# Optimization experiments

Measured on AMD Instinct MI355X. Metric: run time of the kernel, lower is better.

The kernel has to match this reference:

```python
import jax, jax.numpy as jnp
import numpy as np

N_NODES = 100000
N_EDGES = 3200000
NFEAT = 128
NHID = 128
NCLASS = 8
BN_EPS = 1e-5


def setup_inputs() -> dict:
    key = jax.random.key(0)
    ks = jax.random.split(key, 8)
    x = jax.random.normal(ks[0], (N_NODES, NFEAT), dtype=jnp.float32)
    edge_index = jax.random.randint(ks[1], (2, N_EDGES), 0, N_NODES, dtype=jnp.int64)
    # GCNConv params: weight [nfeat, nhid] (glorot), bias [nhid]
    lim = float(np.sqrt(6.0 / (NFEAT + NHID)))
    W = jax.random.uniform(ks[2], (NFEAT, NHID), minval=-lim, maxval=lim, dtype=jnp.float32)
    b_gc = jnp.zeros((NHID,), dtype=jnp.float32)
    # BatchNorm1d params
    gamma = jnp.ones((NHID,), dtype=jnp.float32)
    beta = jnp.zeros((NHID,), dtype=jnp.float32)
    # fc head: (nhid/2) -> nclass, xavier_uniform, zero bias
    lim2 = float(np.sqrt(6.0 / (NHID // 2 + NCLASS)))
    fc_w = jax.random.uniform(ks[3], (NCLASS, NHID // 2), minval=-lim2, maxval=lim2, dtype=jnp.float32)
    fc_b = jnp.zeros((NCLASS,), dtype=jnp.float32)
    return {"x": x, "edge_index": edge_index, "W": W, "b_gc": b_gc,
            "gamma": gamma, "beta": beta, "fc_w": fc_w, "fc_b": fc_b}


def _gcn_conv(x, edge_index, W, b):
    """PyG GCNConv: add self-loops, symmetric norm, linear, gather-scatter, bias."""
    N = x.shape[0]
    loops = jnp.arange(N, dtype=edge_index.dtype)
    src = jnp.concatenate([edge_index[0], loops])  # source (row / x_j)
    dst = jnp.concatenate([edge_index[1], loops])  # target (col / aggregation index)
    # degree of target nodes (edge weight = 1)
    deg = jax.ops.segment_sum(jnp.ones_like(dst, dtype=x.dtype), dst, num_segments=N)
    dinv = jnp.where(deg > 0, jax.lax.rsqrt(deg), 0.0)
    norm = dinv[src] * dinv[dst]  # [E+N]
    h = x @ W  # [N, nhid]
    msg = h[src] * norm[:, None]  # gather + scale
    out = jax.ops.segment_sum(msg, dst, num_segments=N)  # scatter-add
    return out + b


def _batchnorm(h, gamma, beta):
    mean = jnp.mean(h, axis=0)
    var = jnp.mean(jnp.square(h - mean), axis=0)  # biased, training-mode
    return gamma * (h - mean) * jax.lax.rsqrt(var + BN_EPS) + beta


def reference(x, edge_index, W, b_gc, gamma, beta, fc_w, fc_b):
    h = _gcn_conv(x, edge_index, W, b_gc)
    embed = _batchnorm(h, gamma, beta)
    half = embed.shape[1] // 2
    out = embed[:, :half] @ fc_w.T + fc_b
    return (out, embed)
```

## Files before the change

kernel.cpp:

```cpp
#include <hip/hip_runtime.h>
#include <hip/hip_bf16.h>
#include <math.h>

#define N_NODES 100000
#define N_EDGES 3200000
#define NFEAT 128
#define NHID 128
#define NCLASS 8
#define BN_EPS 1e-5f
#define NBC 391
#define PART_BLOCKS 782
#define WT_BLOCKS 64

typedef __attribute__((ext_vector_type(8))) short short8;
typedef __attribute__((ext_vector_type(4))) float f32x4;

__device__ __forceinline__ short f2bf(float f) {
    __hip_bfloat16 b = __float2bfloat16(f);
    return *reinterpret_cast<short*>(&b);
}
__device__ __forceinline__ float bf_lo(unsigned u) { return __uint_as_float(u << 16); }
__device__ __forceinline__ float bf_hi(unsigned u) { return __uint_as_float(u & 0xffff0000u); }


__global__ __launch_bounds__(256) void k_chist(const int* __restrict__ dst,
                                               int* __restrict__ ghist,
                                               const float* __restrict__ W,
                                               unsigned short* __restrict__ Wt,
                                               uint4* __restrict__ hbz) {
    if (blockIdx.x >= PART_BLOCKS) {
        int idx = (blockIdx.x - PART_BLOCKS) * 256 + threadIdx.x;
        if (idx < 16) hbz[idx] = (uint4){0u, 0u, 0u, 0u};
        int k = idx >> 7, n = idx & 127;
        Wt[n * NFEAT + k] = (unsigned short)f2bf(W[idx]);
        return;
    }
    __shared__ int lh[NBC];
    const int tid = threadIdx.x;
    for (int i = tid; i < NBC; i += 256) lh[i] = 0;
    __syncthreads();
    const int4* dst4 = (const int4*)dst;
    const int q0 = blockIdx.x * 1024 + tid;
#pragma unroll
    for (int i = 0; i < 4; ++i) {
        int q = q0 + i * 256;
        if (q < N_EDGES / 4) {
            int4 d = dst4[q];
            atomicAdd(&lh[d.x >> 8], 1);
            atomicAdd(&lh[d.y >> 8], 1);
            atomicAdd(&lh[d.z >> 8], 1);
            atomicAdd(&lh[d.w >> 8], 1);
        }
    }
    __syncthreads();
    for (int i = tid; i < NBC; i += 256) {
        int c = lh[i];
        if (c) atomicAdd(&ghist[i], c);
    }
}

__global__ __launch_bounds__(512) void k_cscan(const int* __restrict__ ghist,
                                               int* __restrict__ coff,
                                               int* __restrict__ ccur,
                                               int* __restrict__ off,
                                               float* __restrict__ stats,
                                               int* __restrict__ ticket) {
    __shared__ int tmp[512];
    const int t = threadIdx.x;
    if (t < 256) stats[t] = 0.f;
    if (t == 0) *ticket = 0;
    int v = (t < NBC) ? ghist[t] : 0;
    tmp[t] = v;
    __syncthreads();
    for (int d = 1; d < 512; d <<= 1) {
        int u = (t >= d) ? tmp[t - d] : 0;
        __syncthreads();
        tmp[t] += u;
        __syncthreads();
    }
    int excl = tmp[t] - v;
    if (t < NBC) {
        coff[t] = excl;
        ccur[t] = excl;
    }
    if (t == NBC - 1) {
        coff[NBC] = tmp[t];
        off[N_NODES] = tmp[t];
    }
}

__global__ __launch_bounds__(256) void k_part(const int* __restrict__ src,
                                              const int* __restrict__ dst,
                                              int* __restrict__ ccur,
                                              unsigned* __restrict__ epack) {
    __shared__ int lh[NBC];
    __shared__ int lbase[NBC];
    const int tid = threadIdx.x;
    for (int i = tid; i < NBC; i += 256) lh[i] = 0;
    __syncthreads();
    const int4* src4 = (const int4*)src;
    const int4* dst4 = (const int4*)dst;
    const int q0 = blockIdx.x * 1024 + tid;
    int4 sv[4], dv[4];
    int rk[16];
    bool val[4];
#pragma unroll
    for (int i = 0; i < 4; ++i) {
        int q = q0 + i * 256;
        val[i] = q < N_EDGES / 4;
        if (val[i]) {
            sv[i] = src4[q];
            dv[i] = dst4[q];
            rk[i * 4 + 0] = atomicAdd(&lh[dv[i].x >> 8], 1);
            rk[i * 4 + 1] = atomicAdd(&lh[dv[i].y >> 8], 1);
            rk[i * 4 + 2] = atomicAdd(&lh[dv[i].z >> 8], 1);
            rk[i * 4 + 3] = atomicAdd(&lh[dv[i].w >> 8], 1);
        }
    }
    __syncthreads();
    for (int i = tid; i < NBC; i += 256) {
        int c = lh[i];
        lbase[i] = c ? atomicAdd(&ccur[i], c) : 0;
    }
    __syncthreads();
#pragma unroll
    for (int i = 0; i < 4; ++i) {
        if (val[i]) {
            epack[lbase[dv[i].x >> 8] + rk[i * 4 + 0]] = ((unsigned)sv[i].x << 8) | (unsigned)(dv[i].x & 255);
            epack[lbase[dv[i].y >> 8] + rk[i * 4 + 1]] = ((unsigned)sv[i].y << 8) | (unsigned)(dv[i].y & 255);
            epack[lbase[dv[i].z >> 8] + rk[i * 4 + 2]] = ((unsigned)sv[i].z << 8) | (unsigned)(dv[i].z & 255);
            epack[lbase[dv[i].w >> 8] + rk[i * 4 + 3]] = ((unsigned)sv[i].w << 8) | (unsigned)(dv[i].w & 255);
        }
    }
}

__global__ __launch_bounds__(256) void k_fine(const unsigned* __restrict__ epack,
                                              const int* __restrict__ coff,
                                              int* __restrict__ off,
                                              float* __restrict__ dinv,
                                              int* __restrict__ esrc) {
    __shared__ int lh[256], lcur[256], lsc[256];
    const int tid = threadIdx.x;
    const int b = blockIdx.x;
    const int node0 = b << 8;
    const int span = min(256, N_NODES - node0);
    lh[tid] = 0;
    __syncthreads();
    const int lo = coff[b], hiEnd = coff[b + 1];
    for (int i = lo + tid; i < hiEnd; i += 256)
        atomicAdd(&lh[epack[i] & 255u], 1);
    __syncthreads();
    int v = lh[tid];
    lsc[tid] = v;
    __syncthreads();
    for (int d = 1; d < 256; d <<= 1) {
        int u = (tid >= d) ? lsc[tid - d] : 0;
        __syncthreads();
        lsc[tid] += u;
        __syncthreads();
    }
    int excl = lsc[tid] - v;
    lcur[tid] = excl;
    if (tid < span) {
        off[node0 + tid] = lo + excl;
        dinv[node0 + tid] = rsqrtf((float)(v + 1));
    }
    __syncthreads();
    for (int i = lo + tid; i < hiEnd; i += 256) {
        unsigned p = epack[i];
        int pos = atomicAdd(&lcur[p & 255u], 1);
        esrc[lo + pos] = (int)(p >> 8);
    }
}


#define WSTRIDE 136
__global__ __launch_bounds__(256) void k_gemm(const float* __restrict__ x,
                                              const unsigned short* __restrict__ Wt,
                                              const float* __restrict__ dinv,
                                              unsigned short* __restrict__ hb) {
    __shared__ short wlds[NHID * WSTRIDE];
    const int tid = threadIdx.x;

    const unsigned* Wt32 = (const unsigned*)Wt;
    unsigned* wl32 = (unsigned*)wlds;
#pragma unroll
    for (int i = 0; i < 32; ++i) {
        int d = tid + i * 256;
        int n = d >> 6, kp = d & 63;
        wl32[n * (WSTRIDE / 2) + kp] = Wt32[d];
    }
    __syncthreads();

    const int wid = tid >> 6, lane = tid & 63;
    const int qw = lane >> 4, lr = lane & 15;
    const int arow = blockIdx.x * 64 + wid * 16 + lr;
    const bool avalid = arow < N_NODES;

    short8 a[4];
#pragma unroll
    for (int ks = 0; ks < 4; ++ks) {
        if (avalid) {
            const float* p = x + (size_t)arow * NFEAT + ks * 32 + qw * 8;
            float4 v0 = *(const float4*)p;
            float4 v1 = *(const float4*)(p + 4);
            short8 t;
            t[0] = f2bf(v0.x); t[1] = f2bf(v0.y); t[2] = f2bf(v0.z); t[3] = f2bf(v0.w);
            t[4] = f2bf(v1.x); t[5] = f2bf(v1.y); t[6] = f2bf(v1.z); t[7] = f2bf(v1.w);
            a[ks] = t;
        } else {
            short8 t;
#pragma unroll
            for (int j = 0; j < 8; ++j) t[j] = 0;
            a[ks] = t;
        }
    }

    f32x4 acc[8];
#pragma unroll
    for (int nt = 0; nt < 8; ++nt) acc[nt] = (f32x4){0.f, 0.f, 0.f, 0.f};

#pragma unroll
    for (int nt = 0; nt < 8; ++nt) {
#pragma unroll
        for (int ks = 0; ks < 4; ++ks) {
            short8 bfr = *(const short8*)&wlds[(nt * 16 + lr) * WSTRIDE + ks * 32 + qw * 8];
            acc[nt] = __builtin_amdgcn_mfma_f32_16x16x32_bf16(a[ks], bfr, acc[nt], 0, 0, 0);
        }
    }

    const int rbase = blockIdx.x * 64 + wid * 16 + qw * 4;
    float dv[4];
#pragma unroll
    for (int j = 0; j < 4; ++j) dv[j] = (rbase + j < N_NODES) ? dinv[rbase + j] : 0.f;
#pragma unroll
    for (int j = 0; j < 4; ++j) {
        int r = rbase + j;
        if (r >= N_NODES) continue;
#pragma unroll
        for (int nt = 0; nt < 8; ++nt)
            hb[(size_t)r * NHID + nt * 16 + lr] = (unsigned short)f2bf(dv[j] * acc[nt][j]);
    }
}


__global__ __launch_bounds__(256) void k_agg(const int* __restrict__ off,
                                             const int* __restrict__ esrc,
                                             const float* __restrict__ dinv,
                                             const uint2* __restrict__ hbq,
                                             float4* __restrict__ agg4) {
    const int node = (blockIdx.x << 2) | (threadIdx.x >> 6);
    const int lane = threadIdx.x & 63;
    const int hl = lane >> 5;
    const int cl = lane & 31;
    if (node >= N_NODES) return;

    const float dn = dinv[node];
    const int self = hl ? N_NODES : node;
    uint2 u0 = hbq[(size_t)self * 32 + cl];
    float aAx = bf_lo(u0.x), aAy = bf_hi(u0.x), aAz = bf_lo(u0.y), aAw = bf_hi(u0.y);
    float aBx = 0.f, aBy = 0.f, aBz = 0.f, aBw = 0.f;
    float aCx = 0.f, aCy = 0.f, aCz = 0.f, aCw = 0.f;
    float aDx = 0.f, aDy = 0.f, aDz = 0.f, aDw = 0.f;

    const int begin = off[node], end = off[node + 1];
    for (int base = begin; base < end; base += 64) {
        int m = end - base;
        if (m > 64) m = 64;
        int sv = (lane < m) ? esrc[base + lane] : N_NODES;
        const int kmax = (m + 7) >> 3;
        for (int k = 0; k < kmax; ++k) {
            int sA = __shfl(sv, 8 * k + 0 + hl);
            int sB = __shfl(sv, 8 * k + 2 + hl);
            int sC = __shfl(sv, 8 * k + 4 + hl);
            int sD = __shfl(sv, 8 * k + 6 + hl);
            uint2 uA = hbq[(size_t)sA * 32 + cl];
            uint2 uB = hbq[(size_t)sB * 32 + cl];
            uint2 uC = hbq[(size_t)sC * 32 + cl];
            uint2 uD = hbq[(size_t)sD * 32 + cl];
            aAx += bf_lo(uA.x); aAy += bf_hi(uA.x); aAz += bf_lo(uA.y); aAw += bf_hi(uA.y);
            aBx += bf_lo(uB.x); aBy += bf_hi(uB.x); aBz += bf_lo(uB.y); aBw += bf_hi(uB.y);
            aCx += bf_lo(uC.x); aCy += bf_hi(uC.x); aCz += bf_lo(uC.y); aCw += bf_hi(uC.y);
            aDx += bf_lo(uD.x); aDy += bf_hi(uD.x); aDz += bf_lo(uD.y); aDw += bf_hi(uD.y);
        }
    }
    float ax = (aAx + aBx) + (aCx + aDx);
    float ay = (aAy + aBy) + (aCy + aDy);
    float az = (aAz + aBz) + (aCz + aDz);
    float aw = (aAw + aBw) + (aCw + aDw);
    ax += __shfl_xor(ax, 32);
    ay += __shfl_xor(ay, 32);
    az += __shfl_xor(az, 32);
    aw += __shfl_xor(aw, 32);
    if (hl == 0) {
        float4 o;
        o.x = ax * dn; o.y = ay * dn; o.z = az * dn; o.w = aw * dn;
        agg4[(size_t)node * 32 + cl] = o;
    }
}


__global__ __launch_bounds__(256) void k_stats(const float* __restrict__ agg,
                                               float* __restrict__ stats,
                                               int* __restrict__ ticket,
                                               const float* __restrict__ gamma,
                                               const float* __restrict__ beta,
                                               float* __restrict__ ss) {
    const int cb = threadIdx.x & 31;
    const int rg = threadIdx.x >> 5;
    const float4* a4 = (const float4*)agg;
    float4 s = {0.f, 0.f, 0.f, 0.f}, s2 = {0.f, 0.f, 0.f, 0.f};
    for (int r = blockIdx.x * 8 + rg; r < N_NODES; r += gridDim.x * 8) {
        float4 v = a4[(size_t)r * 32 + cb];
        s.x += v.x; s.y += v.y; s.z += v.z; s.w += v.w;
        s2.x += v.x * v.x; s2.y += v.y * v.y; s2.z += v.z * v.z; s2.w += v.w * v.w;
    }
    __shared__ float4 ls[256], ls2[256];
    __shared__ int lastflag;
    ls[threadIdx.x] = s;
    ls2[threadIdx.x] = s2;
    __syncthreads();
    if (rg == 0) {
        float4 ts = ls[cb], t2 = ls2[cb];
#pragma unroll
        for (int g = 1; g < 8; ++g) {
            float4 v = ls[g * 32 + cb], w = ls2[g * 32 + cb];
            ts.x += v.x; ts.y += v.y; ts.z += v.z; ts.w += v.w;
            t2.x += w.x; t2.y += w.y; t2.z += w.z; t2.w += w.w;
        }
        atomicAdd(&stats[cb * 4 + 0], ts.x);
        atomicAdd(&stats[cb * 4 + 1], ts.y);
        atomicAdd(&stats[cb * 4 + 2], ts.z);
        atomicAdd(&stats[cb * 4 + 3], ts.w);
        atomicAdd(&stats[128 + cb * 4 + 0], t2.x);
        atomicAdd(&stats[128 + cb * 4 + 1], t2.y);
        atomicAdd(&stats[128 + cb * 4 + 2], t2.z);
        atomicAdd(&stats[128 + cb * 4 + 3], t2.w);
    }
    __threadfence();
    __syncthreads();
    if (threadIdx.x == 0)
        lastflag = (atomicAdd(ticket, 1) == (int)gridDim.x - 1) ? 1 : 0;
    __syncthreads();
    if (lastflag && threadIdx.x < NHID) {
        int c = threadIdx.x;
        float sum = atomicAdd(&stats[c], 0.f);
        float sq  = atomicAdd(&stats[128 + c], 0.f);
        float mean = sum / (float)N_NODES;
        float var = fmaxf(sq / (float)N_NODES - mean * mean, 0.f);
        float inv = rsqrtf(var + BN_EPS);
        float sc = gamma[c] * inv;
        ss[c] = sc;
        ss[128 + c] = beta[c] - mean * sc;
    }
}


__global__ __launch_bounds__(256) void k_bnfc(float* __restrict__ embed,
                                              const float* __restrict__ ss,
                                              const float* __restrict__ fc_w,
                                              const float* __restrict__ fc_b,
                                              float* __restrict__ out) {
    __shared__ float se[64][68];
    __shared__ float sw[8][68];
    __shared__ float sb[8];
    const int tid = threadIdx.x;
    const int row0 = blockIdx.x * 64;
    {
        int d = tid;
        sw[d >> 6][d & 63] = fc_w[d];
        d = tid + 256;
        sw[d >> 6][d & 63] = fc_w[d];
        if (tid < 8) sb[tid] = fc_b[tid];
    }
    float4* ef4 = (float4*)embed;
    const float4* ssc4 = (const float4*)ss;
    const float4* ssh4 = (const float4*)(ss + 128);
#pragma unroll
    for (int i = 0; i < 8; ++i) {
        int d = tid + i * 256;
        int r = d >> 5;
        int cb = d & 31;
        int gr = row0 + r;
        if (gr < N_NODES) {
            float4 v = ef4[(size_t)gr * 32 + cb];
            float4 sc = ssc4[cb], sh = ssh4[cb];
            v.x = fmaf(v.x, sc.x, sh.x);
            v.y = fmaf(v.y, sc.y, sh.y);
            v.z = fmaf(v.z, sc.z, sh.z);
            v.w = fmaf(v.w, sc.w, sh.w);
            ef4[(size_t)gr * 32 + cb] = v;
            if (cb < 16) {
                se[r][cb * 4 + 0] = v.x; se[r][cb * 4 + 1] = v.y;
                se[r][cb * 4 + 2] = v.z; se[r][cb * 4 + 3] = v.w;
            }
        } else if (cb < 16) {
            se[r][cb * 4 + 0] = 0.f; se[r][cb * 4 + 1] = 0.f;
            se[r][cb * 4 + 2] = 0.f; se[r][cb * 4 + 3] = 0.f;
        }
    }
    __syncthreads();
    const int r = tid >> 2;
    const int j0 = (tid & 3) * 2;
    const int gr = row0 + r;
#pragma unroll
    for (int jj = 0; jj < 2; ++jj) {
        int j = j0 + jj;
        float s = sb[j];
#pragma unroll
        for (int k = 0; k < 64; ++k) s = fmaf(se[r][k], sw[j][k], s);
        if (gr < N_NODES) out[(size_t)gr * NCLASS + j] = s;
    }
}


extern "C" void kernel_launch(void* const* d_in, const int* in_sizes, int n_in,
                              void* d_out, int out_size, void* d_ws, size_t ws_size,
                              hipStream_t stream) {
    const float* x     = (const float*)d_in[0];
    const int*   ei    = (const int*)d_in[1];
    const float* W     = (const float*)d_in[2];
    const float* gamma = (const float*)d_in[4];
    const float* beta  = (const float*)d_in[5];
    const float* fc_w  = (const float*)d_in[6];
    const float* fc_b  = (const float*)d_in[7];

    const int* src = ei;
    const int* dst = ei + N_EDGES;

    float* out   = (float*)d_out;
    float* embed = (float*)d_out + (size_t)N_NODES * NCLASS;

    char* ws = (char*)d_ws;
    size_t o = 0;
    unsigned* epack = (unsigned*)(ws + o);          o += (size_t)N_EDGES * 4;
    unsigned short* hb = (unsigned short*)(ws + o); o += (size_t)(N_NODES + 1) * NHID * 2;
    o = (o + 255) & ~(size_t)255;
    int* esrc   = (int*)(ws + o);                   o += (size_t)N_EDGES * 4;
    int* off    = (int*)(ws + o);                   o += (size_t)(N_NODES + 1) * 4;
    float* dinv = (float*)(ws + o);                 o += (size_t)N_NODES * 4;
    unsigned short* Wt = (unsigned short*)(ws + o); o += (size_t)NFEAT * NHID * 2;
    float* stats = (float*)(ws + o);                o += 256 * 4;
    float* ss    = (float*)(ws + o);                o += 256 * 4;
    int* ghist   = (int*)(ws + o);                  o += NBC * 4;
    int* coff    = (int*)(ws + o);                  o += (NBC + 1) * 4;
    int* ccur    = (int*)(ws + o);                  o += NBC * 4;
    int* ticket  = (int*)(ws + o);                  o += 4;

    hipMemsetAsync(ghist, 0, NBC * 4, stream);

    k_chist<<<PART_BLOCKS + WT_BLOCKS, 256, 0, stream>>>(dst, ghist, W, Wt,
                                                         (uint4*)(hb + (size_t)N_NODES * NHID));
    k_cscan<<<1, 512, 0, stream>>>(ghist, coff, ccur, off, stats, ticket);
    k_part<<<PART_BLOCKS, 256, 0, stream>>>(src, dst, ccur, epack);
    k_fine<<<NBC, 256, 0, stream>>>(epack, coff, off, dinv, esrc);

    k_gemm<<<(N_NODES + 63) / 64, 256, 0, stream>>>(x, Wt, dinv, hb);

    k_agg<<<(N_NODES + 3) / 4, 256, 0, stream>>>(off, esrc, dinv, (const uint2*)hb, (float4*)embed);

    k_stats<<<512, 256, 0, stream>>>(embed, stats, ticket, gamma, beta, ss);

    k_bnfc<<<(N_NODES + 63) / 64, 256, 0, stream>>>(embed, ss, fc_w, fc_b, out);
}
```

Baseline: 321.2 us.

## Split feature matrix into 16-column slices so aggregation gathers stay cache-resident

The GEMM now writes h in eight column-slice planes of 16 bf16 features each. The aggregation kernel is reorganized so each block handles one slice for 8 nodes, with each wave gathering only 32-byte rows. The aim is to shrink the random-gather working set per slice (about 3.2 MB) so it fits in L2/LLC, improving hit rate on the 3.2M-edge gather. The cost is that the edge list is re-read eight times (with nontemporal loads) and outputs are written as strided scalar stores. Block-to-slice interleaving sets the order in which slices run.

```diff
diff --git a/kernel.cpp b/kernel.cpp
--- a/kernel.cpp
+++ b/kernel.cpp
@@ -11,6 +11,7 @@
 #define NBC 391
 #define PART_BLOCKS 782
 #define WT_BLOCKS 64
+#define PSTRIDE_U ((N_NODES + 16) * 16)
 
 typedef __attribute__((ext_vector_type(8))) short short8;
 typedef __attribute__((ext_vector_type(4))) float f32x4;
@@ -27,10 +28,13 @@
                                                int* __restrict__ ghist,
                                                const float* __restrict__ W,
                                                unsigned short* __restrict__ Wt,
-                                               uint4* __restrict__ hbz) {
+                                               unsigned short* __restrict__ hbS) {
     if (blockIdx.x >= PART_BLOCKS) {
         int idx = (blockIdx.x - PART_BLOCKS) * 256 + threadIdx.x;
-        if (idx < 16) hbz[idx] = (uint4){0u, 0u, 0u, 0u};
+        if (idx < 128) {
+            int s = idx >> 4, e = idx & 15;
+            hbS[(size_t)s * PSTRIDE_U + (size_t)N_NODES * 16 + e] = 0;
+        }
         int k = idx >> 7, n = idx & 127;
         Wt[n * NFEAT + k] = (unsigned short)f2bf(W[idx]);
         return;
@@ -178,7 +182,7 @@
 __global__ __launch_bounds__(256) void k_gemm(const float* __restrict__ x,
                                               const unsigned short* __restrict__ Wt,
                                               const float* __restrict__ dinv,
-                                              unsigned short* __restrict__ hb) {
+                                              unsigned short* __restrict__ hbS) {
     __shared__ short wlds[NHID * WSTRIDE];
     const int tid = threadIdx.x;
 
@@ -239,63 +243,55 @@
         if (r >= N_NODES) continue;
 #pragma unroll
         for (int nt = 0; nt < 8; ++nt)
-            hb[(size_t)r * NHID + nt * 16 + lr] = (unsigned short)f2bf(dv[j] * acc[nt][j]);
-    }
-}
-
-
-__global__ __launch_bounds__(256) void k_agg(const int* __restrict__ off,
+            hbS[(size_t)nt * PSTRIDE_U + (size_t)r * 16 + lr] = (unsigned short)f2bf(dv[j] * acc[nt][j]);
+    }
+}
+
+
+__global__ __launch_bounds__(512) void k_agg(const int* __restrict__ off,
                                              const int* __restrict__ esrc,
                                              const float* __restrict__ dinv,
-                                             const uint2* __restrict__ hbq,
-                                             float4* __restrict__ agg4) {
-    const int node = (blockIdx.x << 2) | (threadIdx.x >> 6);
+                                             const unsigned* __restrict__ hbS32,
+                                             float* __restrict__ embed) {
+    const int slice = blockIdx.x & 7;
+    const int chunk = blockIdx.x >> 3;
+    const int wv = threadIdx.x >> 6;
     const int lane = threadIdx.x & 63;
-    const int hl = lane >> 5;
-    const int cl = lane & 31;
-    if (node >= N_NODES) return;
-
-    const float dn = dinv[node];
-    const int self = hl ? N_NODES : node;
-    uint2 u0 = hbq[(size_t)self * 32 + cl];
-    float aAx = bf_lo(u0.x), aAy = bf_hi(u0.x), aAz = bf_lo(u0.y), aAw = bf_hi(u0.y);
-    float aBx = 0.f, aBy = 0.f, aBz = 0.f, aBw = 0.f;
-    float aCx = 0.f, aCy = 0.f, aCz = 0.f, aCw = 0.f;
-    float aDx = 0.f, aDy = 0.f, aDz = 0.f, aDw = 0.f;
+    const int grp = lane >> 3, gl = lane & 7;
+    const int node = chunk * 8 + wv;
+
+    const unsigned* __restrict__ hp = hbS32 + (size_t)slice * (PSTRIDE_U / 2);
+
+    unsigned u0 = (grp == 0) ? hp[(size_t)node * 8 + gl] : 0u;
+    float aAx = bf_lo(u0), aAy = bf_hi(u0);
+    float aBx = 0.f, aBy = 0.f;
 
     const int begin = off[node], end = off[node + 1];
     for (int base = begin; base < end; base += 64) {
         int m = end - base;
         if (m > 64) m = 64;
-        int sv = (lane < m) ? esrc[base + lane] : N_NODES;
+        int sv = (lane < m) ? __builtin_nontemporal_load(esrc + base + lane) : N_NODES;
         const int kmax = (m + 7) >> 3;
-        for (int k = 0; k < kmax; ++k) {
-            int sA = __shfl(sv, 8 * k + 0 + hl);
-            int sB = __shfl(sv, 8 * k + 2 + hl);
-            int sC = __shfl(sv, 8 * k + 4 + hl);
-            int sD = __shfl(sv, 8 * k + 6 + hl);
-            uint2 uA = hbq[(size_t)sA * 32 + cl];
-            uint2 uB = hbq[(size_t)sB * 32 + cl];
-            uint2 uC = hbq[(size_t)sC * 32 + cl];
-            uint2 uD = hbq[(size_t)sD * 32 + cl];
-            aAx += bf_lo(uA.x); aAy += bf_hi(uA.x); aAz += bf_lo(uA.y); aAw += bf_hi(uA.y);
-            aBx += bf_lo(uB.x); aBy += bf_hi(uB.x); aBz += bf_lo(uB.y); aBw += bf_hi(uB.y);
-            aCx += bf_lo(uC.x); aCy += bf_hi(uC.x); aCz += bf_lo(uC.y); aCw += bf_hi(uC.y);
-            aDx += bf_lo(uD.x); aDy += bf_hi(uD.x); aDz += bf_lo(uD.y); aDw += bf_hi(uD.y);
-        }
-    }
-    float ax = (aAx + aBx) + (aCx + aDx);
-    float ay = (aAy + aBy) + (aCy + aDy);
-    float az = (aAz + aBz) + (aCz + aDz);
-    float aw = (aAw + aBw) + (aCw + aDw);
-    ax += __shfl_xor(ax, 32);
-    ay += __shfl_xor(ay, 32);
-    az += __shfl_xor(az, 32);
-    aw += __shfl_xor(aw, 32);
-    if (hl == 0) {
-        float4 o;
-        o.x = ax * dn; o.y = ay * dn; o.z = az * dn; o.w = aw * dn;
-        agg4[(size_t)node * 32 + cl] = o;
+        for (int k = 0; k < kmax; k += 2) {
+            int sA = __shfl(sv, 8 * k + grp);
+            int sB = __shfl(sv, 8 * k + 8 + grp);
+            unsigned uA = hp[(size_t)sA * 8 + gl];
+            unsigned uB = hp[(size_t)sB * 8 + gl];
+            aAx += bf_lo(uA); aAy += bf_hi(uA);
+            aBx += bf_lo(uB); aBy += bf_hi(uB);
+        }
+    }
+    float ax = aAx + aBx, ay = aAy + aBy;
+#pragma unroll
+    for (int d = 8; d < 64; d <<= 1) {
+        ax += __shfl_xor(ax, d);
+        ay += __shfl_xor(ay, d);
+    }
+    if (grp == 0) {
+        const float dn = dinv[node];
+        float* ep = embed + (size_t)node * NHID + slice * 16 + gl * 2;
+        __builtin_nontemporal_store(ax * dn, ep);
+        __builtin_nontemporal_store(ay * dn, ep + 1);
     }
 }
 
@@ -434,7 +430,7 @@
     char* ws = (char*)d_ws;
     size_t o = 0;
     unsigned* epack = (unsigned*)(ws + o);          o += (size_t)N_EDGES * 4;
-    unsigned short* hb = (unsigned short*)(ws + o); o += (size_t)(N_NODES + 1) * NHID * 2;
+    unsigned short* hbS = (unsigned short*)(ws + o); o += (size_t)8 * PSTRIDE_U * 2;
     o = (o + 255) & ~(size_t)255;
     int* esrc   = (int*)(ws + o);                   o += (size_t)N_EDGES * 4;
     int* off    = (int*)(ws + o);                   o += (size_t)(N_NODES + 1) * 4;
@@ -449,15 +445,14 @@
 
     hipMemsetAsync(ghist, 0, NBC * 4, stream);
 
-    k_chist<<<PART_BLOCKS + WT_BLOCKS, 256, 0, stream>>>(dst, ghist, W, Wt,
-                                                         (uint4*)(hb + (size_t)N_NODES * NHID));
+    k_chist<<<PART_BLOCKS + WT_BLOCKS, 256, 0, stream>>>(dst, ghist, W, Wt, hbS);
     k_cscan<<<1, 512, 0, stream>>>(ghist, coff, ccur, off, stats, ticket);
     k_part<<<PART_BLOCKS, 256, 0, stream>>>(src, dst, ccur, epack);
     k_fine<<<NBC, 256, 0, stream>>>(epack, coff, off, dinv, esrc);
 
-    k_gemm<<<(N_NODES + 63) / 64, 256, 0, stream>>>(x, Wt, dinv, hb);
-
-    k_agg<<<(N_NODES + 3) / 4, 256, 0, stream>>>(off, esrc, dinv, (const uint2*)hb, (float4*)embed);
+    k_gemm<<<(N_NODES + 63) / 64, 256, 0, stream>>>(x, Wt, dinv, hbS);
+
+    k_agg<<<8 * (N_NODES / 8), 512, 0, stream>>>(off, esrc, dinv, (const unsigned*)hbS, embed);
 
     k_stats<<<512, 256, 0, stream>>>(embed, stats, ticket, gamma, beta, ss);
 
```

New measurement: 479.2 us. +49.2%, slower.

## Stage partitioned edges in LDS and widen coarse buckets to 512 nodes

Applied to the files above, without the earlier changes.

The coarse partition now uses 512-node buckets (196 buckets) and 8192 edges per block. Each block sorts its edges locally in shared memory by bucket, using an in-block scan, before writing them to global memory. The goal is to turn scattered 4-byte global writes into mostly contiguous runs per bucket and to halve the number of global atomics on the bucket cursors. The cost is more LDS per block (about 48KB), which lowers occupancy, plus extra scans and syncs; the fine pass also has to handle 512 nodes per block.

```diff
diff --git a/kernel.cpp b/kernel.cpp
--- a/kernel.cpp
+++ b/kernel.cpp
@@ -8,8 +8,10 @@
 #define NHID 128
 #define NCLASS 8
 #define BN_EPS 1e-5f
-#define NBC 391
-#define PART_BLOCKS 782
+#define CB 512
+#define NBC 196
+#define EPB 8192
+#define PART_BLOCKS 391
 #define WT_BLOCKS 64
 
 typedef __attribute__((ext_vector_type(8))) short short8;
@@ -37,25 +39,25 @@
     }
     __shared__ int lh[NBC];
     const int tid = threadIdx.x;
-    for (int i = tid; i < NBC; i += 256) lh[i] = 0;
+    if (tid < NBC) lh[tid] = 0;
     __syncthreads();
     const int4* dst4 = (const int4*)dst;
-    const int q0 = blockIdx.x * 1024 + tid;
-#pragma unroll
-    for (int i = 0; i < 4; ++i) {
+    const int q0 = blockIdx.x * (EPB / 4) + tid;
+#pragma unroll
+    for (int i = 0; i < 8; ++i) {
         int q = q0 + i * 256;
         if (q < N_EDGES / 4) {
             int4 d = dst4[q];
-            atomicAdd(&lh[d.x >> 8], 1);
-            atomicAdd(&lh[d.y >> 8], 1);
-            atomicAdd(&lh[d.z >> 8], 1);
-            atomicAdd(&lh[d.w >> 8], 1);
-        }
-    }
-    __syncthreads();
-    for (int i = tid; i < NBC; i += 256) {
-        int c = lh[i];
-        if (c) atomicAdd(&ghist[i], c);
+            atomicAdd(&lh[d.x >> 9], 1);
+            atomicAdd(&lh[d.y >> 9], 1);
+            atomicAdd(&lh[d.z >> 9], 1);
+            atomicAdd(&lh[d.w >> 9], 1);
+        }
+    }
+    __syncthreads();
+    if (tid < NBC) {
+        int c = lh[tid];
+        if (c) atomicAdd(&ghist[tid], c);
     }
 }
 
@@ -89,69 +91,93 @@
     }
 }
 
+
 __global__ __launch_bounds__(256) void k_part(const int* __restrict__ src,
                                               const int* __restrict__ dst,
                                               int* __restrict__ ccur,
                                               unsigned* __restrict__ epack) {
     __shared__ int lh[NBC];
-    __shared__ int lbase[NBC];
+    __shared__ int lstart[NBC];
+    __shared__ int adj[NBC];
+    __shared__ int stmp[256];
+    __shared__ unsigned sorted[EPB];
+    __shared__ unsigned short bkt[EPB];
     const int tid = threadIdx.x;
-    for (int i = tid; i < NBC; i += 256) lh[i] = 0;
+    if (tid < NBC) lh[tid] = 0;
     __syncthreads();
     const int4* src4 = (const int4*)src;
     const int4* dst4 = (const int4*)dst;
-    const int q0 = blockIdx.x * 1024 + tid;
-    int4 sv[4], dv[4];
-    int rk[16];
-    bool val[4];
-#pragma unroll
-    for (int i = 0; i < 4; ++i) {
+    const int q0 = blockIdx.x * (EPB / 4) + tid;
+    int4 sv[8], dv[8];
+    int rk[32];
+#pragma unroll
+    for (int i = 0; i < 8; ++i) {
         int q = q0 + i * 256;
-        val[i] = q < N_EDGES / 4;
-        if (val[i]) {
+        if (q < N_EDGES / 4) {
             sv[i] = src4[q];
             dv[i] = dst4[q];
-            rk[i * 4 + 0] = atomicAdd(&lh[dv[i].x >> 8], 1);
-            rk[i * 4 + 1] = atomicAdd(&lh[dv[i].y >> 8], 1);
-            rk[i * 4 + 2] = atomicAdd(&lh[dv[i].z >> 8], 1);
-            rk[i * 4 + 3] = atomicAdd(&lh[dv[i].w >> 8], 1);
-        }
-    }
-    __syncthreads();
-    for (int i = tid; i < NBC; i += 256) {
-        int c = lh[i];
-        lbase[i] = c ? atomicAdd(&ccur[i], c) : 0;
-    }
-    __syncthreads();
-#pragma unroll
-    for (int i = 0; i < 4; ++i) {
-        if (val[i]) {
-            epack[lbase[dv[i].x >> 8] + rk[i * 4 + 0]] = ((unsigned)sv[i].x << 8) | (unsigned)(dv[i].x & 255);
-            epack[lbase[dv[i].y >> 8] + rk[i * 4 + 1]] = ((unsigned)sv[i].y << 8) | (unsigned)(dv[i].y & 255);
-            epack[lbase[dv[i].z >> 8] + rk[i * 4 + 2]] = ((unsigned)sv[i].z << 8) | (unsigned)(dv[i].z & 255);
-            epack[lbase[dv[i].w >> 8] + rk[i * 4 + 3]] = ((unsigned)sv[i].w << 8) | (unsigned)(dv[i].w & 255);
-        }
-    }
-}
+            rk[i * 4 + 0] = atomicAdd(&lh[dv[i].x >> 9], 1);
+            rk[i * 4 + 1] = atomicAdd(&lh[dv[i].y >> 9], 1);
+            rk[i * 4 + 2] = atomicAdd(&lh[dv[i].z >> 9], 1);
+            rk[i * 4 + 3] = atomicAdd(&lh[dv[i].w >> 9], 1);
+        } else dv[i].x = -1;
+    }
+    __syncthreads();
+    int v = (tid < NBC) ? lh[tid] : 0;
+    stmp[tid] = v;
+    __syncthreads();
+    for (int d = 1; d < 256; d <<= 1) {
+        int u = (tid >= d) ? stmp[tid - d] : 0;
+        __syncthreads();
+        stmp[tid] += u;
+        __syncthreads();
+    }
+    if (tid < NBC) {
+        int ls = stmp[tid] - v;
+        lstart[tid] = ls;
+        adj[tid] = (v ? atomicAdd(&ccur[tid], v) : 0) - ls;
+    }
+    __syncthreads();
+#pragma unroll
+    for (int i = 0; i < 8; ++i) {
+        if (dv[i].x >= 0) {
+            int b, p;
+            b = dv[i].x >> 9; p = lstart[b] + rk[i * 4 + 0];
+            sorted[p] = ((unsigned)sv[i].x << 9) | (unsigned)(dv[i].x & 511); bkt[p] = (unsigned short)b;
+            b = dv[i].y >> 9; p = lstart[b] + rk[i * 4 + 1];
+            sorted[p] = ((unsigned)sv[i].y << 9) | (unsigned)(dv[i].y & 511); bkt[p] = (unsigned short)b;
+            b = dv[i].z >> 9; p = lstart[b] + rk[i * 4 + 2];
+            sorted[p] = ((unsigned)sv[i].z << 9) | (unsigned)(dv[i].z & 511); bkt[p] = (unsigned short)b;
+            b = dv[i].w >> 9; p = lstart[b] + rk[i * 4 + 3];
+            sorted[p] = ((unsigned)sv[i].w << 9) | (unsigned)(dv[i].w & 511); bkt[p] = (unsigned short)b;
+        }
+    }
+    __syncthreads();
+    const int vcnt = stmp[255];
+    for (int p = tid; p < vcnt; p += 256)
+        epack[p + adj[bkt[p]]] = sorted[p];
+}
+
 
 __global__ __launch_bounds__(256) void k_fine(const unsigned* __restrict__ epack,
                                               const int* __restrict__ coff,
                                               int* __restrict__ off,
                                               float* __restrict__ dinv,
                                               int* __restrict__ esrc) {
-    __shared__ int lh[256], lcur[256], lsc[256];
+    __shared__ int lh[CB], lcur[CB], lsc[256];
     const int tid = threadIdx.x;
     const int b = blockIdx.x;
-    const int node0 = b << 8;
-    const int span = min(256, N_NODES - node0);
+    const int node0 = b << 9;
     lh[tid] = 0;
+    lh[tid + 256] = 0;
     __syncthreads();
     const int lo = coff[b], hiEnd = coff[b + 1];
     for (int i = lo + tid; i < hiEnd; i += 256)
-        atomicAdd(&lh[epack[i] & 255u], 1);
-    __syncthreads();
-    int v = lh[tid];
-    lsc[tid] = v;
+        atomicAdd(&lh[epack[i] & 511u], 1);
+    __syncthreads();
+    int v0 = lh[2 * tid], v1 = lh[2 * tid + 1];
+    int s = v0 + v1;
+    lsc[tid] = s;
     __syncthreads();
     for (int d = 1; d < 256; d <<= 1) {
         int u = (tid >= d) ? lsc[tid - d] : 0;
@@ -159,17 +185,17 @@
         lsc[tid] += u;
         __syncthreads();
     }
-    int excl = lsc[tid] - v;
-    lcur[tid] = excl;
-    if (tid < span) {
-        off[node0 + tid] = lo + excl;
-        dinv[node0 + tid] = rsqrtf((float)(v + 1));
-    }
+    int pairExcl = lsc[tid] - s;
+    lcur[2 * tid] = pairExcl;
+    lcur[2 * tid + 1] = pairExcl + v0;
+    int n0 = node0 + 2 * tid, n1 = n0 + 1;
+    if (n0 < N_NODES) { off[n0] = lo + pairExcl;      dinv[n0] = rsqrtf((float)(v0 + 1)); }
+    if (n1 < N_NODES) { off[n1] = lo + pairExcl + v0; dinv[n1] = rsqrtf((float)(v1 + 1)); }
     __syncthreads();
     for (int i = lo + tid; i < hiEnd; i += 256) {
         unsigned p = epack[i];
-        int pos = atomicAdd(&lcur[p & 255u], 1);
-        esrc[lo + pos] = (int)(p >> 8);
+        int pos = atomicAdd(&lcur[p & 511u], 1);
+        esrc[lo + pos] = (int)(p >> 9);
     }
 }
 
```

Result: faster. 314.3 us (-2.1%).
